# Performance work log

Hardware: AMD Instinct MI355X
Metric: run time of the kernel (lower is better)

Reference implementation:

```python
import jax, jax.numpy as jnp
import numpy as np

B, L, C = 128, 512, 321
PRED = 336
S = 4
K = 25  # moving_avg kernel
EPS = 1e-5
N = L // S          # 128
H = 2048 // S       # 512


def setup_inputs() -> dict:
    key = jax.random.key(0)
    ks = jax.random.split(key, 16)
    def w(k, shape, fan_in):
        return jax.random.uniform(k, shape, jnp.float32, -1.0, 1.0) / np.sqrt(fan_in)
    return {
        "x": jax.random.normal(ks[0], (B, L, C), jnp.float32),
        "revin_w": jnp.ones((C,), jnp.float32),
        "revin_b": jnp.zeros((C,), jnp.float32),
        "W11": w(ks[1], (N, H), N), "b11": w(ks[2], (H,), N),
        "W12": w(ks[3], (H, N), H), "b12": w(ks[4], (N,), H),
        "W21": w(ks[5], (N, H), N), "b21": w(ks[6], (H,), N),
        "W22": w(ks[7], (H, N), H), "b22": w(ks[8], (N,), H),
        "W_tr": w(ks[9], (L, PRED), L), "b_tr": w(ks[10], (PRED,), L),
        "W_se": w(ks[11], (L, PRED), L), "b_se": w(ks[12], (PRED,), L),
    }


def reference(x, revin_w, revin_b, W11, b11, W12, b12, W21, b21, W22, b22,
              W_tr, b_tr, W_se, b_se):
    # RevIN norm (statistics are detached in the original)
    mean = jax.lax.stop_gradient(jnp.mean(x, axis=1, keepdims=True))
    std = jax.lax.stop_gradient(
        jnp.sqrt(jnp.var(x, axis=1, keepdims=True) + EPS))
    xn = (x - mean) / std * revin_w + revin_b  # [B, L, C]

    # Decomp: replicate-pad along time then moving average of width K
    front = jnp.repeat(xn[:, 0:1, :], K - 1 - (K - 1) // 2, axis=1)
    end = jnp.repeat(xn[:, -1:, :], (K - 1) // 2, axis=1)
    padded = jnp.concatenate([front, xn, end], axis=1)  # [B, L+K-1, C]
    cs = jnp.concatenate(
        [jnp.zeros((B, 1, C), padded.dtype), jnp.cumsum(padded, axis=1)], axis=1)
    trend = (cs[:, K:, :] - cs[:, :-K, :]) / K  # [B, L, C]
    seasonal = xn - trend

    trend_p = jnp.transpose(trend, (0, 2, 1))      # [B, C, L]
    seasonal_p = jnp.transpose(seasonal, (0, 2, 1))  # [B, C, L]

    # Trend head: Linear L -> PRED
    trend_out = jnp.einsum('bcl,lp->bcp', trend_p, W_tr) + b_tr

    # Seasonal head: Splitting (strided interleave) = reshape + transpose
    xs = seasonal_p.reshape(B, C, N, S).transpose(0, 1, 3, 2)  # [B, C, S, N]
    h = jnp.matmul(jax.nn.gelu(jnp.matmul(xs, W11) + b11, approximate=False), W12) + b12
    h = jnp.matmul(jax.nn.gelu(jnp.matmul(h, W21) + b21, approximate=False), W22) + b22
    # Catting is the exact inverse interleave
    sea = h.transpose(0, 1, 3, 2).reshape(B, C, L)  # [B, C, L]
    sea_out = jnp.einsum('bcl,lp->bcp', sea, W_se) + b_se

    out = jnp.transpose(trend_out + sea_out, (0, 2, 1))  # [B, PRED, C]

    # RevIN denorm
    out = (out - revin_b) / (revin_w + EPS * EPS)
    out = out * std + mean
    return out
```

## Files before the change

kernel.cpp:

```cpp
#include <hip/hip_runtime.h>
#include <math.h>

#define BB   128
#define LL   512
#define CC   321
#define PREDD 336

using bf16x8  = __attribute__((ext_vector_type(8))) __bf16;
using floatx4 = __attribute__((ext_vector_type(4))) float;
using uintx4  = __attribute__((ext_vector_type(4))) unsigned int;
typedef unsigned short u16;
typedef unsigned int u32;

#define MFMA16(a,b,c) __builtin_amdgcn_mfma_f32_16x16x32_bf16(a,b,c,0,0,0)

__device__ __forceinline__ u16 f2bf(float f){
    union { float f; unsigned u; } v; v.f = f;
    unsigned r = v.u + 0x7FFFu + ((v.u >> 16) & 1u);
    return (u16)(r >> 16);
}

__device__ __forceinline__ float fgelu(float x){
    float u = x*(0.7978845608f + 0.035677408f*x*x);
    float a = fminf(u*2.8853900818f, 80.f);
    float t = __builtin_amdgcn_exp2f(a);
    return x*t*__builtin_amdgcn_rcpf(1.f + t);
}

__device__ __forceinline__ int swz128(int r, int s){ return r*128 + (((s & 8) | ((s ^ r) & 7)) << 3); }
__device__ __forceinline__ int swz64 (int r, int s){ return r*64  + (((s ^ r) & 7) << 3); }

__device__ __forceinline__ void dma16(const u16* g, const u16* l){
    __builtin_amdgcn_global_load_lds(
        (const __attribute__((address_space(1))) u32*)g,
        (__attribute__((address_space(3))) u32*)l, 16, 0, 0);
}

__global__ void prep_k(const float* __restrict__ W11, const float* __restrict__ W12,
                       const float* __restrict__ W21, const float* __restrict__ W22,
                       const float* __restrict__ Wtr, const float* __restrict__ Wse,
                       u16* __restrict__ BT1, u16* __restrict__ BT2,
                       u16* __restrict__ BT3, u16* __restrict__ BT4,
                       u16* __restrict__ BT5)
{
    int idx = blockIdx.x * 256 + threadIdx.x;
    if (idx < 65536){
        int h = idx >> 7, k = idx & 127;
        BT1[idx] = f2bf(W11[k*512 + h]);
        BT3[idx] = f2bf(W21[k*512 + h]);
        int n = idx >> 9, k2 = idx & 511;
        BT2[idx] = f2bf(W12[k2*128 + n]);
        BT4[idx] = f2bf(W22[k2*128 + n]);
    }
    if (idx < 393216){
        int p = idx >> 10, k = idx & 1023;
        float v = 0.f;
        if (p < PREDD){
            if (k < 512) v = Wtr[k*PREDD + p];
            else { int kk = k - 512; int s = kk >> 7; int n = kk & 127; v = Wse[(4*n + s)*PREDD + p]; }
        }
        BT5[idx] = f2bf(v);
    }
}

#define XT(t,c) xt[((t)<<4) + (((t)>>5)<<1) + (c)]
__global__ __launch_bounds__(256) void decomp_k(
    const float* __restrict__ x, const float* __restrict__ rw, const float* __restrict__ rb,
    u16* __restrict__ Afin, u16* __restrict__ xs, float2* __restrict__ stats)
{
    __shared__ float xt[8240];
    __shared__ float red[2][16][16];
    __shared__ float sh_m[16], sh_istd[16];
    int b = blockIdx.x / 21, ct = blockIdx.x % 21;
    int tid = threadIdx.x;

    int cl = tid & 15, lp = tid >> 4;
    int c = ct*16 + cl;
    bool valid = c < CC;
    const float* xb = x + (size_t)b*LL*CC;
    float s = 0.f, q = 0.f;
    for (int i = 0; i < 32; ++i){
        int t = lp + 16*i;
        float v = valid ? xb[(size_t)t*CC + c] : 0.f;
        XT(t, cl) = v;
        s += v; q += v*v;
    }
    red[0][lp][cl] = s; red[1][lp][cl] = q;
    __syncthreads();
    if (tid < 16){
        float ss = 0.f, qq = 0.f;
        for (int j = 0; j < 16; ++j){ ss += red[0][j][tid]; qq += red[1][j][tid]; }
        float m  = ss * (1.f/512.f);
        float var = qq * (1.f/512.f) - m*m;
        float sd = sqrtf(var + 1e-5f);
        sh_m[tid] = m; sh_istd[tid] = 1.f/sd;
        int cc = ct*16 + tid;
        if (cc < CC) stats[(size_t)b*CC + cc] = make_float2(m, sd);
    }
    __syncthreads();

    int ch = tid >> 4, tp = tid & 15;
    int c2 = ct*16 + ch;
    if (c2 >= CC) return;
    float m = sh_m[ch], istd = sh_istd[ch];
    float w = rw[c2] * istd, bbv = rb[c2];
    size_t bc = (size_t)b*CC + c2;
    u16* tr  = Afin + bc*1024;
    u16* xsr = xs   + bc*512;
    int t0 = tp*32;

    float win = 0.f;
#pragma unroll
    for (int d = -12; d <= 12; ++d){
        int u = t0 + d; u = u < 0 ? 0 : (u > 511 ? 511 : u);
        win += XT(u, ch);
    }
    u16 trbuf[8];
    u16 xsbuf[4][8];
#pragma unroll
    for (int i = 0; i < 32; ++i){
        int t = t0 + i;
        float Ax = win * (1.f/25.f);
        float xv = XT(t, ch);
        trbuf[i & 7] = f2bf((Ax - m)*w + bbv);
        xsbuf[i & 3][i >> 2] = f2bf((xv - Ax)*w);
        if ((i & 7) == 7)
            *(uintx4*)(tr + t0 + (i & ~7)) = *(const uintx4*)trbuf;
        int uo = t - 12; uo = uo < 0 ? 0 : uo;
        int un = t + 13; un = un > 511 ? 511 : un;
        win += XT(un, ch) - XT(uo, ch);
    }
#pragma unroll
    for (int s4 = 0; s4 < 4; ++s4)
        *(uintx4*)(xsr + s4*128 + tp*8) = *(const uintx4*)xsbuf[s4];
}

#define SL1 16384
#define HS  32768
__global__ __launch_bounds__(256, 2) void mlp_fused_k(
    const u16* __restrict__ xs,
    const u16* __restrict__ BT1, const float* __restrict__ b11,
    const u16* __restrict__ BT2, const float* __restrict__ b12,
    const u16* __restrict__ BT3, const float* __restrict__ b21,
    const u16* __restrict__ BT4, const float* __restrict__ b22,
    u16* __restrict__ Afin)
{
    __shared__ u16 lds[40960];
    const int tid = threadIdx.x;
    const int row0 = blockIdx.x * 128;
    const int lane = tid & 63;
    const int wv = tid >> 6;
    const int quad = lane >> 4, cl = lane & 15;
    const int wrow = row0 + wv*32;
    u16* hscr = lds + HS + wv*2048;
    const int rdswz = ((cl >> 2) & 3) << 4;

#pragma unroll
    for (int i = 0; i < 4; ++i){
        int qq = (wv*4 + i)*64 + lane;
        { int r = qq >> 4, sp = qq & 15; int s = (sp & 8) | ((sp ^ r) & 7);
          dma16(BT1 + (size_t)r*128 + s*8, lds + qq*8); }
        { int r = qq >> 3, p = qq & 7; int s = (p ^ r) & 7;
          dma16(BT2 + (size_t)r*512 + s*8, lds + 8192 + qq*8); }
    }
    bf16x8 afrag[2][4];
#pragma unroll
    for (int mt = 0; mt < 2; ++mt)
#pragma unroll
        for (int ks = 0; ks < 4; ++ks)
            afrag[mt][ks] = *(const bf16x8*)(xs + (size_t)(wrow + mt*16 + cl)*128 + ks*32 + quad*8);

    floatx4 Yacc[16];
#pragma unroll
    for (int i = 0; i < 16; ++i) Yacc[i] = (floatx4){0.f,0.f,0.f,0.f};

    __syncthreads();

    for (int g = 0; g < 16; ++g){
        const int cur = (g & 1) ? SL1 : 0;
        const int nxt = (g & 1) ? 0 : SL1;
        if (g < 15){
            const u16* w1s = ((g+1) & 8) ? BT3 : BT1;
            const u16* w2s = ((g+1) & 8) ? BT4 : BT2;
            const int hb = ((g+1) & 7) * 64;
#pragma unroll
            for (int i = 0; i < 4; ++i){
                int qq = (wv*4 + i)*64 + lane;
                { int r = qq >> 4, sp = qq & 15; int s = (sp & 8) | ((sp ^ r) & 7);
                  dma16(w1s + (size_t)(hb + r)*128 + s*8, lds + nxt + qq*8); }
                { int r = qq >> 3, p = qq & 7; int s = (p ^ r) & 7;
                  dma16(w2s + (size_t)r*512 + hb + s*8, lds + nxt + 8192 + qq*8); }
            }
        }
        const float* ba = (g & 8) ? b21 : b11;
        const int hc = g & 7;

        floatx4 hacc[8];
#pragma unroll
        for (int i = 0; i < 8; ++i) hacc[i] = (floatx4){0.f,0.f,0.f,0.f};
#pragma unroll
        for (int ks = 0; ks < 4; ++ks){
            bf16x8 bfr[4];
#pragma unroll
            for (int nt = 0; nt < 4; ++nt)
                bfr[nt] = *(const bf16x8*)(lds + cur + swz128(nt*16 + cl, ks*4 + quad));
#pragma unroll
            for (int mt = 0; mt < 2; ++mt)
#pragma unroll
                for (int nt = 0; nt < 4; ++nt)
                    hacc[mt*4+nt] = MFMA16(afrag[mt][ks], bfr[nt], hacc[mt*4+nt]);
        }
#pragma unroll
        for (int mt = 0; mt < 2; ++mt)
#pragma unroll
            for (int nt = 0; nt < 4; ++nt){
                floatx4 v = hacc[mt*4+nt];
                int h = nt*16 + cl;
                float bav = ba[hc*64 + h];
#pragma unroll
                for (int i = 0; i < 4; ++i){
                    int r = mt*16 + quad*4 + i;
                    hscr[r*64 + (h ^ (quad << 4))] = f2bf(fgelu(v[i] + bav));
                }
            }
#pragma unroll
        for (int ks = 0; ks < 2; ++ks){
            bf16x8 a2[2];
#pragma unroll
            for (int mt = 0; mt < 2; ++mt)
                a2[mt] = *(const bf16x8*)(hscr + (mt*16 + cl)*64 + ((ks*32 + quad*8) ^ rdswz));
#pragma unroll
            for (int nt = 0; nt < 8; ++nt){
                bf16x8 b2 = *(const bf16x8*)(lds + cur + 8192 + swz64(nt*16 + cl, ks*4 + quad));
#pragma unroll
                for (int mt = 0; mt < 2; ++mt)
                    Yacc[mt*8+nt] = MFMA16(a2[mt], b2, Yacc[mt*8+nt]);
            }
        }
        __syncthreads();

        if (g == 7){
#pragma unroll
            for (int half = 0; half < 2; ++half){
#pragma unroll
                for (int mt = 0; mt < 2; ++mt)
#pragma unroll
                    for (int nt = 0; nt < 4; ++nt){
                        int ntg = half*4 + nt;
                        floatx4 v = Yacc[mt*8+ntg];
                        int c = ntg*16 + cl;
                        float bv = b12[c];
                        int h = nt*16 + cl;
#pragma unroll
                        for (int i = 0; i < 4; ++i){
                            int r = mt*16 + quad*4 + i;
                            hscr[r*64 + (h ^ (quad << 4))] = f2bf(v[i] + bv);
                        }
                    }
#pragma unroll
                for (int mt = 0; mt < 2; ++mt)
#pragma unroll
                    for (int k2 = 0; k2 < 2; ++k2)
                        afrag[mt][half*2 + k2] = *(const bf16x8*)(hscr + (mt*16 + cl)*64 + ((k2*32 + quad*8) ^ rdswz));
            }
#pragma unroll
            for (int i = 0; i < 16; ++i) Yacc[i] = (floatx4){0.f,0.f,0.f,0.f};
        }
    }

#pragma unroll
    for (int mt = 0; mt < 2; ++mt)
#pragma unroll
        for (int nt = 0; nt < 8; ++nt){
            int c = nt*16 + cl;
            float bv = b22[c];
            floatx4 v = Yacc[mt*8+nt];
#pragma unroll
            for (int i = 0; i < 4; ++i){
                int gr = wrow + mt*16 + quad*4 + i;
                Afin[(size_t)(gr>>2)*1024 + 512 + (size_t)(gr&3)*128 + c] = f2bf(v[i] + bv);
            }
        }
}

__global__ __launch_bounds__(256, 2) void head_gemm_k(
    const u16* __restrict__ A, const u16* __restrict__ BT,
    float* __restrict__ Cf,
    const float* __restrict__ bias, const float* __restrict__ bias2,
    const float* __restrict__ rw, const float* __restrict__ rb,
    const float2* __restrict__ stats)
{
    __shared__ u16 lds[32768];
    const int id = blockIdx.x;
    const int xcd = id & 7, slot = id >> 3;
    const int g8 = slot / 3, j = slot - g8*3;
    const int by = xcd + 8*g8;
    if (by >= 321) return;
    const int row0 = by * 128, col0 = j * 128;

    const int tid = threadIdx.x;
    const int lane = tid & 63;
    const int wv = tid >> 6;
    const int wm = wv & 1, wn = wv >> 1;
    const int quad = lane >> 4, cl = lane & 15;

    const int qbase = wv*4*64 + lane;

#pragma unroll
    for (int i = 0; i < 4; ++i){
        int qq = qbase + i*64;
        int r = qq >> 3, p = qq & 7; int s = (p ^ r) & 7;
        dma16(A  + (size_t)(row0 + r)*1024 + s*8, lds + qq*8);
        dma16(BT + (size_t)(col0 + r)*1024 + s*8, lds + 16384 + qq*8);
    }
    __syncthreads();

    floatx4 acc[16];
#pragma unroll
    for (int i = 0; i < 16; ++i) acc[i] = (floatx4){0.f,0.f,0.f,0.f};

    for (int it = 0; it < 16; ++it){
        const int cur = (it & 1) * 8192;
        if (it < 15){
            const int nxt = ((it+1) & 1) * 8192;
            const int k0 = (it+1) * 64;
#pragma unroll
            for (int i = 0; i < 4; ++i){
                int qq = qbase + i*64;
                int r = qq >> 3, p = qq & 7; int s = (p ^ r) & 7;
                dma16(A  + (size_t)(row0 + r)*1024 + k0 + s*8, lds + nxt + qq*8);
                dma16(BT + (size_t)(col0 + r)*1024 + k0 + s*8, lds + 16384 + nxt + qq*8);
            }
        }
#pragma unroll
        for (int kk = 0; kk < 2; ++kk){
            bf16x8 af[4], bfr[4];
#pragma unroll
            for (int mt = 0; mt < 4; ++mt) af[mt]  = *(const bf16x8*)(lds + cur + swz64(wm*64 + mt*16 + cl, kk*4 + quad));
#pragma unroll
            for (int nt = 0; nt < 4; ++nt) bfr[nt] = *(const bf16x8*)(lds + 16384 + cur + swz64(wn*64 + nt*16 + cl, kk*4 + quad));
#pragma unroll
            for (int mt = 0; mt < 4; ++mt)
#pragma unroll
                for (int nt = 0; nt < 4; ++nt)
                    acc[mt*4+nt] = MFMA16(af[mt], bfr[nt], acc[mt*4+nt]);
        }
        __syncthreads();
    }

#pragma unroll
    for (int mt = 0; mt < 4; ++mt)
#pragma unroll
        for (int nt = 0; nt < 4; ++nt){
            floatx4 v = acc[mt*4+nt];
            int gc = col0 + wn*64 + nt*16 + cl;
            if (gc >= PREDD) continue;
            float bsum = bias[gc] + bias2[gc];
#pragma unroll
            for (int i = 0; i < 4; ++i){
                int gr = row0 + wm*64 + mt*16 + quad*4 + i;
                float val = v[i] + bsum;
                int bv2 = gr / CC;
                int c  = gr - bv2*CC;
                val = (val - rb[c]) / (rw[c] + 1e-10f);
                float2 st = stats[gr];
                val = val*st.y + st.x;
                Cf[(size_t)bv2*(PREDD*CC) + (size_t)gc*CC + c] = val;
            }
        }
}

extern "C" void kernel_launch(void* const* d_in, const int* in_sizes, int n_in,
                              void* d_out, int out_size, void* d_ws, size_t ws_size,
                              hipStream_t stream)
{
    const float* x   = (const float*)d_in[0];
    const float* rvw = (const float*)d_in[1];
    const float* rvb = (const float*)d_in[2];
    const float* W11 = (const float*)d_in[3];
    const float* b11 = (const float*)d_in[4];
    const float* W12 = (const float*)d_in[5];
    const float* b12 = (const float*)d_in[6];
    const float* W21 = (const float*)d_in[7];
    const float* b21 = (const float*)d_in[8];
    const float* W22 = (const float*)d_in[9];
    const float* b22 = (const float*)d_in[10];
    const float* Wtr = (const float*)d_in[11];
    const float* btr = (const float*)d_in[12];
    const float* Wse = (const float*)d_in[13];
    const float* bse = (const float*)d_in[14];
    float* out = (float*)d_out;

    char* ws = (char*)d_ws;
    u16* BT1 = (u16*)(ws + 0);
    u16* BT2 = (u16*)(ws + 131072);
    u16* BT3 = (u16*)(ws + 262144);
    u16* BT4 = (u16*)(ws + 393216);
    u16* BT5 = (u16*)(ws + 524288);
    float2* stats = (float2*)(ws + 1310720);
    u16* Afin = (u16*)(ws + 1639424);
    u16* xs   = (u16*)(ws + 85787648);

    hipLaunchKernelGGL(prep_k, dim3(1536), dim3(256), 0, stream,
                       W11, W12, W21, W22, Wtr, Wse, BT1, BT2, BT3, BT4, BT5);
    hipLaunchKernelGGL(decomp_k, dim3(128*21), dim3(256), 0, stream,
                       x, rvw, rvb, Afin, xs, stats);
    hipLaunchKernelGGL(mlp_fused_k, dim3(1284), dim3(256), 0, stream,
                       xs, BT1, b11, BT2, b12, BT3, b21, BT4, b22, Afin);
    hipLaunchKernelGGL(head_gemm_k, dim3(984), dim3(256), 0, stream,
                       Afin, BT5, out, btr, bse, rvw, rvb, stats);
}
```

Before: 469.7 us.

## Restructure fused MLP to keep hidden activations in registers via permuted weights

The fused seasonal MLP kernel now computes transposed MFMA tiles (weights as A, activations as B). The prep kernel permutes W11/W21 columns and W12 rows so the GELU output of the first GEMM lands directly in the register layout needed as the operand of the second GEMM. This removes the per-wave LDS scratch round trip for hidden activations and for the inter-layer handoff. The hidden chunk shrinks from 64 to 32 with 32 iterations, LDS drops to 32KB, occupancy is raised to 3 blocks per CU, and packed bf16 conversion instructions replace scalar rounding. The trade-off is more iterations and barriers, and a correctness risk in the index permutation.

```diff
diff --git a/kernel.cpp b/kernel.cpp
--- a/kernel.cpp
+++ b/kernel.cpp
@@ -18,6 +18,12 @@
     union { float f; unsigned u; } v; v.f = f;
     unsigned r = v.u + 0x7FFFu + ((v.u >> 16) & 1u);
     return (u16)(r >> 16);
+}
+
+__device__ __forceinline__ u32 cvtpk(float a, float b){
+    u32 r;
+    asm("v_cvt_pk_bf16_f32 %0, %1, %2" : "=v"(r) : "v"(a), "v"(b));
+    return r;
 }
 
 __device__ __forceinline__ float fgelu(float x){
@@ -45,11 +51,14 @@
 {
     int idx = blockIdx.x * 256 + threadIdx.x;
     if (idx < 65536){
-        int h = idx >> 7, k = idx & 127;
-        BT1[idx] = f2bf(W11[k*512 + h]);
-        BT3[idx] = f2bf(W21[k*512 + h]);
+        int h = idx >> 7;
+        int k = idx & 127;
+        int hp = (h & ~31) | (((h >> 2) & 3)*8 + ((h >> 4) & 1)*4 + (h & 3));
+        BT1[idx] = f2bf(W11[k*512 + hp]);
+        BT3[idx] = f2bf(W21[k*512 + hp]);
         int n = idx >> 9, k2 = idx & 511;
-        BT2[idx] = f2bf(W12[k2*128 + n]);
+        int np = ((n >> 5) & 3)*32 + ((n >> 2) & 3)*8 + ((n >> 4) & 1)*4 + (n & 3);
+        BT2[idx] = f2bf(W12[k2*128 + np]);
         BT4[idx] = f2bf(W22[k2*128 + n]);
     }
     if (idx < 393216){
@@ -135,9 +144,7 @@
         *(uintx4*)(xsr + s4*128 + tp*8) = *(const uintx4*)xsbuf[s4];
 }
 
-#define SL1 16384
-#define HS  32768
-__global__ __launch_bounds__(256, 2) void mlp_fused_k(
+__global__ __launch_bounds__(256, 3) void mlp_fused_k(
     const u16* __restrict__ xs,
     const u16* __restrict__ BT1, const float* __restrict__ b11,
     const u16* __restrict__ BT2, const float* __restrict__ b12,
@@ -145,30 +152,37 @@
     const u16* __restrict__ BT4, const float* __restrict__ b22,
     u16* __restrict__ Afin)
 {
-    __shared__ u16 lds[40960];
-    const int tid = threadIdx.x;
-    const int row0 = blockIdx.x * 128;
+    __shared__ u16 lds[16384];
+    const int tid  = threadIdx.x;
     const int lane = tid & 63;
-    const int wv = tid >> 6;
+    const int wv   = tid >> 6;
     const int quad = lane >> 4, cl = lane & 15;
-    const int wrow = row0 + wv*32;
-    u16* hscr = lds + HS + wv*2048;
-    const int rdswz = ((cl >> 2) & 3) << 4;
-
-#pragma unroll
-    for (int i = 0; i < 4; ++i){
-        int qq = (wv*4 + i)*64 + lane;
-        { int r = qq >> 4, sp = qq & 15; int s = (sp & 8) | ((sp ^ r) & 7);
-          dma16(BT1 + (size_t)r*128 + s*8, lds + qq*8); }
-        { int r = qq >> 3, p = qq & 7; int s = (p ^ r) & 7;
-          dma16(BT2 + (size_t)r*512 + s*8, lds + 8192 + qq*8); }
-    }
-    bf16x8 afrag[2][4];
+    const int wrow = blockIdx.x * 128 + wv * 32;
+
+    const int qq0 = tid, qq1 = tid + 256;
+    const int rA0 = qq0 >> 4, spA0 = qq0 & 15;
+    const int rA1 = qq1 >> 4, spA1 = qq1 & 15;
+    const int offA0 = rA0*128 + (((spA0 & 8) | ((spA0 ^ rA0) & 7)) << 3);
+    const int offA1 = rA1*128 + (((spA1 & 8) | ((spA1 ^ rA1) & 7)) << 3);
+    const int rB0 = qq0 >> 2, spB0 = qq0 & 3;
+    const int rB1 = qq1 >> 2, spB1 = qq1 & 3;
+    const int offB0 = rB0*512 + ((spB0 ^ ((rB0 >> 1) & 3)) << 3);
+    const int offB1 = rB1*512 + ((spB1 ^ ((rB1 >> 1) & 3)) << 3);
+
+#define STAGE(dst, w1, w2, hcc)                                          \
+    dma16((w1) + (hcc)*4096 + offA0, lds + (dst) + qq0*8);               \
+    dma16((w1) + (hcc)*4096 + offA1, lds + (dst) + qq1*8);               \
+    dma16((w2) + (hcc)*32  + offB0, lds + (dst) + 4096 + qq0*8);         \
+    dma16((w2) + (hcc)*32  + offB1, lds + (dst) + 4096 + qq1*8);
+
+    STAGE(0, BT1, BT2, 0)
+
+    bf16x8 xfrag[2][4];
 #pragma unroll
     for (int mt = 0; mt < 2; ++mt)
 #pragma unroll
         for (int ks = 0; ks < 4; ++ks)
-            afrag[mt][ks] = *(const bf16x8*)(xs + (size_t)(wrow + mt*16 + cl)*128 + ks*32 + quad*8);
+            xfrag[mt][ks] = *(const bf16x8*)(xs + (size_t)(wrow + mt*16 + cl)*128 + ks*32 + quad*8);
 
     floatx4 Yacc[16];
 #pragma unroll
@@ -176,111 +190,94 @@
 
     __syncthreads();
 
-    for (int g = 0; g < 16; ++g){
-        const int cur = (g & 1) ? SL1 : 0;
-        const int nxt = (g & 1) ? 0 : SL1;
-        if (g < 15){
-            const u16* w1s = ((g+1) & 8) ? BT3 : BT1;
-            const u16* w2s = ((g+1) & 8) ? BT4 : BT2;
-            const int hb = ((g+1) & 7) * 64;
-#pragma unroll
-            for (int i = 0; i < 4; ++i){
-                int qq = (wv*4 + i)*64 + lane;
-                { int r = qq >> 4, sp = qq & 15; int s = (sp & 8) | ((sp ^ r) & 7);
-                  dma16(w1s + (size_t)(hb + r)*128 + s*8, lds + nxt + qq*8); }
-                { int r = qq >> 3, p = qq & 7; int s = (p ^ r) & 7;
-                  dma16(w2s + (size_t)r*512 + hb + s*8, lds + nxt + 8192 + qq*8); }
+    const int w2rd = (quad ^ ((cl >> 1) & 3)) << 3;
+
+    for (int g = 0; g < 32; ++g){
+        const int cur = (g & 1) ? 8192 : 0;
+        if (g < 31){
+            const int nxt = 8192 - cur;
+            const u16* w1s = ((g+1) & 16) ? BT3 : BT1;
+            const u16* w2s = ((g+1) & 16) ? BT4 : BT2;
+            const int hn = (g+1) & 15;
+            STAGE(nxt, w1s, w2s, hn)
+        }
+        const float* ba = (g & 16) ? b21 : b11;
+        const int hc = g & 15;
+
+        floatx4 hacc[2][2];
+        hacc[0][0] = hacc[0][1] = hacc[1][0] = hacc[1][1] = (floatx4){0.f,0.f,0.f,0.f};
+#pragma unroll
+        for (int ks = 0; ks < 4; ++ks){
+            const int sg = ks*4 + quad;
+            const int s0 = ((sg & 8) | ((sg ^ cl) & 7)) << 3;
+            bf16x8 wf0 = *(const bf16x8*)(lds + cur + cl*128 + s0);
+            bf16x8 wf1 = *(const bf16x8*)(lds + cur + (16 + cl)*128 + s0);
+#pragma unroll
+            for (int mt = 0; mt < 2; ++mt){
+                hacc[0][mt] = MFMA16(wf0, xfrag[mt][ks], hacc[0][mt]);
+                hacc[1][mt] = MFMA16(wf1, xfrag[mt][ks], hacc[1][mt]);
             }
         }
-        const float* ba = (g & 8) ? b21 : b11;
-        const int hc = g & 7;
-
-        floatx4 hacc[8];
-#pragma unroll
-        for (int i = 0; i < 8; ++i) hacc[i] = (floatx4){0.f,0.f,0.f,0.f};
-#pragma unroll
-        for (int ks = 0; ks < 4; ++ks){
-            bf16x8 bfr[4];
-#pragma unroll
-            for (int nt = 0; nt < 4; ++nt)
-                bfr[nt] = *(const bf16x8*)(lds + cur + swz128(nt*16 + cl, ks*4 + quad));
+
+        const float4 bA = *(const float4*)(ba + hc*32 + quad*8);
+        const float4 bB = *(const float4*)(ba + hc*32 + quad*8 + 4);
+        bf16x8 a2[2];
+#pragma unroll
+        for (int mt = 0; mt < 2; ++mt){
+            union { bf16x8 v; u32 w[4]; } u;
+            u.w[0] = cvtpk(fgelu(hacc[0][mt][0] + bA.x), fgelu(hacc[0][mt][1] + bA.y));
+            u.w[1] = cvtpk(fgelu(hacc[0][mt][2] + bA.z), fgelu(hacc[0][mt][3] + bA.w));
+            u.w[2] = cvtpk(fgelu(hacc[1][mt][0] + bB.x), fgelu(hacc[1][mt][1] + bB.y));
+            u.w[3] = cvtpk(fgelu(hacc[1][mt][2] + bB.z), fgelu(hacc[1][mt][3] + bB.w));
+            a2[mt] = u.v;
+        }
+
+#pragma unroll
+        for (int nt2 = 0; nt2 < 8; ++nt2){
+            bf16x8 b2 = *(const bf16x8*)(lds + cur + 4096 + (nt2*16 + cl)*32 + w2rd);
 #pragma unroll
             for (int mt = 0; mt < 2; ++mt)
-#pragma unroll
-                for (int nt = 0; nt < 4; ++nt)
-                    hacc[mt*4+nt] = MFMA16(afrag[mt][ks], bfr[nt], hacc[mt*4+nt]);
-        }
-#pragma unroll
-        for (int mt = 0; mt < 2; ++mt)
-#pragma unroll
-            for (int nt = 0; nt < 4; ++nt){
-                floatx4 v = hacc[mt*4+nt];
-                int h = nt*16 + cl;
-                float bav = ba[hc*64 + h];
-#pragma unroll
-                for (int i = 0; i < 4; ++i){
-                    int r = mt*16 + quad*4 + i;
-                    hscr[r*64 + (h ^ (quad << 4))] = f2bf(fgelu(v[i] + bav));
+                Yacc[mt*8 + nt2] = MFMA16(b2, a2[mt], Yacc[mt*8 + nt2]);
+        }
+        __syncthreads();
+
+        if (g == 15){
+#pragma unroll
+            for (int ks = 0; ks < 4; ++ks){
+                const float4 cA = *(const float4*)(b12 + ks*32 + quad*8);
+                const float4 cB = *(const float4*)(b12 + ks*32 + quad*8 + 4);
+#pragma unroll
+                for (int mt = 0; mt < 2; ++mt){
+                    floatx4 y0 = Yacc[mt*8 + 2*ks];
+                    floatx4 y1 = Yacc[mt*8 + 2*ks + 1];
+                    union { bf16x8 v; u32 w[4]; } u;
+                    u.w[0] = cvtpk(y0[0] + cA.x, y0[1] + cA.y);
+                    u.w[1] = cvtpk(y0[2] + cA.z, y0[3] + cA.w);
+                    u.w[2] = cvtpk(y1[0] + cB.x, y1[1] + cB.y);
+                    u.w[3] = cvtpk(y1[2] + cB.z, y1[3] + cB.w);
+                    xfrag[mt][ks] = u.v;
                 }
             }
 #pragma unroll
-        for (int ks = 0; ks < 2; ++ks){
-            bf16x8 a2[2];
-#pragma unroll
-            for (int mt = 0; mt < 2; ++mt)
-                a2[mt] = *(const bf16x8*)(hscr + (mt*16 + cl)*64 + ((ks*32 + quad*8) ^ rdswz));
-#pragma unroll
-            for (int nt = 0; nt < 8; ++nt){
-                bf16x8 b2 = *(const bf16x8*)(lds + cur + 8192 + swz64(nt*16 + cl, ks*4 + quad));
-#pragma unroll
-                for (int mt = 0; mt < 2; ++mt)
-                    Yacc[mt*8+nt] = MFMA16(a2[mt], b2, Yacc[mt*8+nt]);
-            }
-        }
-        __syncthreads();
-
-        if (g == 7){
-#pragma unroll
-            for (int half = 0; half < 2; ++half){
-#pragma unroll
-                for (int mt = 0; mt < 2; ++mt)
-#pragma unroll
-                    for (int nt = 0; nt < 4; ++nt){
-                        int ntg = half*4 + nt;
-                        floatx4 v = Yacc[mt*8+ntg];
-                        int c = ntg*16 + cl;
-                        float bv = b12[c];
-                        int h = nt*16 + cl;
-#pragma unroll
-                        for (int i = 0; i < 4; ++i){
-                            int r = mt*16 + quad*4 + i;
-                            hscr[r*64 + (h ^ (quad << 4))] = f2bf(v[i] + bv);
-                        }
-                    }
-#pragma unroll
-                for (int mt = 0; mt < 2; ++mt)
-#pragma unroll
-                    for (int k2 = 0; k2 < 2; ++k2)
-                        afrag[mt][half*2 + k2] = *(const bf16x8*)(hscr + (mt*16 + cl)*64 + ((k2*32 + quad*8) ^ rdswz));
-            }
-#pragma unroll
             for (int i = 0; i < 16; ++i) Yacc[i] = (floatx4){0.f,0.f,0.f,0.f};
         }
     }
 
 #pragma unroll
-    for (int mt = 0; mt < 2; ++mt)
-#pragma unroll
-        for (int nt = 0; nt < 8; ++nt){
-            int c = nt*16 + cl;
-            float bv = b22[c];
-            floatx4 v = Yacc[mt*8+nt];
-#pragma unroll
-            for (int i = 0; i < 4; ++i){
-                int gr = wrow + mt*16 + quad*4 + i;
-                Afin[(size_t)(gr>>2)*1024 + 512 + (size_t)(gr&3)*128 + c] = f2bf(v[i] + bv);
-            }
-        }
+    for (int mt = 0; mt < 2; ++mt){
+        const int gr = wrow + mt*16 + cl;
+        u16* dst = Afin + (size_t)(gr >> 2)*1024 + 512 + (size_t)(gr & 3)*128 + quad*4;
+#pragma unroll
+        for (int nt2 = 0; nt2 < 8; ++nt2){
+            const float4 cB = *(const float4*)(b22 + nt2*16 + quad*4);
+            floatx4 v = Yacc[mt*8 + nt2];
+            union { unsigned long long d; u32 w[2]; } u;
+            u.w[0] = cvtpk(v[0] + cB.x, v[1] + cB.y);
+            u.w[1] = cvtpk(v[2] + cB.z, v[3] + cB.w);
+            *(unsigned long long*)(dst + nt2*16) = u.d;
+        }
+    }
+#undef STAGE
 }
 
 __global__ __launch_bounds__(256, 2) void head_gemm_k(
```

Result: faster. 432.9 us (-7.8%).
